# Optimization experiments

Hardware: AMD Instinct MI355X
Metric: run time of the kernel (lower is better)

## Reference

```python
import jax, jax.numpy as jnp
import numpy as np
from jax import lax

KS = [3, 3, 3, 5, 5, 7, 7, 7, 9, 9, 11, 11]  # deterministic sorted draw from [3,5,7,9,11], k=12
B, L, OUT_CH = 32, 262144, 4
EPS = 1e-5


def setup_inputs() -> dict:
    key = jax.random.key(0)
    ks = jax.random.split(key, 8 + len(KS))
    inp = {
        "x": jax.random.normal(ks[0], (B, 1, L), jnp.float32),
        "w1": jax.random.normal(ks[1], (128, 256), jnp.float32) * 0.0625,
        "b1": jnp.zeros((128,), jnp.float32),
        "w2": jax.random.normal(ks[2], (12, 128), jnp.float32) * 0.088,
        "b2": jnp.zeros((12,), jnp.float32),
        "bn_gamma": jnp.ones((OUT_CH,), jnp.float32),
        "bn_beta": jnp.zeros((OUT_CH,), jnp.float32),
    }
    for i, k in enumerate(KS):
        inp[f"k{i}"] = jax.random.normal(ks[8 + i], (OUT_CH, 1, k), jnp.float32)
    return inp


def reference(x, w1, b1, w2, b2, bn_gamma, bn_beta,
              k0, k1, k2, k3, k4, k5, k6, k7, k8, k9, k10, k11):
    kernels = [k0, k1, k2, k3, k4, k5, k6, k7, k8, k9, k10, k11]
    b, _, n = x.shape
    # Attention: AdaptiveAvgPool1d(256) -> Linear -> ReLU -> Linear -> softmax(dim=2)
    pooled = x.reshape(b, 1, 256, n // 256).mean(-1)            # [B,1,256]
    h = jax.nn.relu(jnp.einsum('bcd,hd->bch', pooled, w1) + b1)  # [B,1,128]
    y = jax.nn.softmax(jnp.einsum('bch,fh->bcf', h, w2) + b2, axis=2)  # [B,1,12]
    s = y[0, 0]  # scalar weight per filter (faithful to y[0][0][i] in source)

    max_len = n - KS[0] + 1
    out = jnp.zeros((b, OUT_CH, max_len), x.dtype)
    for i, k in enumerate(kernels):
        c = lax.conv_general_dilated(x, k * s[i], (1,), 'VALID',
                                     dimension_numbers=('NCH', 'OIH', 'NCH'))
        out = out.at[:, :, :c.shape[-1]].add(c)  # right-pad-with-zeros then add

    # BatchNorm1d in training mode: batch stats over (N, L), biased variance
    mean = out.mean(axis=(0, 2), keepdims=True)
    var = ((out - mean) ** 2).mean(axis=(0, 2), keepdims=True)
    out = (out - mean) * lax.rsqrt(var + EPS)
    out = out * bn_gamma[None, :, None] + bn_beta[None, :, None]
    return jax.nn.relu(out)
```

## Files before the change

kernel.cpp:

```cpp
#include <hip/hip_runtime.h>

#define L_LEN   262144
#define OUT_LEN 262142
#define BATCH   32
#define NTOT    (32.0 * 262142.0)

typedef float v4f __attribute__((ext_vector_type(4)));

struct KPtrs { const float* p[12]; };

__global__ void pool_kernel(const float* __restrict__ x, float* __restrict__ pooled) {
    int bin = blockIdx.x;
    int tid = threadIdx.x;
    const float4* x4 = (const float4*)(x + bin * 1024);
    float4 v = x4[tid];
    float sum = v.x + v.y + v.z + v.w;
    #pragma unroll
    for (int off = 32; off; off >>= 1) sum += __shfl_down(sum, off);
    __shared__ float wred[4];
    int wave = tid >> 6;
    if ((tid & 63) == 0) wred[wave] = sum;
    __syncthreads();
    if (tid == 0)
        pooled[bin] = (wred[0] + wred[1] + wred[2] + wred[3]) * (1.0f / 1024.0f);
}

__global__ __launch_bounds__(256, 4) void stats_mlp_kernel(const float* __restrict__ x,
                                                           const float* __restrict__ w1,
                                                           const float* __restrict__ b1,
                                                           const float* __restrict__ w2,
                                                           const float* __restrict__ b2,
                                                           KPtrs kp,
                                                           const float* __restrict__ pooled,
                                                           float* __restrict__ part,
                                                           float* __restrict__ Kraw) {
    int tid = threadIdx.x;

    if (blockIdx.x == 0) {
        __shared__ float h[128];
        __shared__ float logits[12];
        __shared__ float s[12];
        int w = tid >> 6, lane = tid & 63;
        float4 pv = ((const float4*)pooled)[lane];
        for (int i = 0; i < 32; ++i) {
            int t = w * 32 + i;
            float4 wv = ((const float4*)(w1 + t * 256))[lane];
            float p = wv.x * pv.x + wv.y * pv.y + wv.z * pv.z + wv.w * pv.w;
            #pragma unroll
            for (int off = 32; off; off >>= 1) p += __shfl_down(p, off);
            if (lane == 0) h[t] = fmaxf(p + b1[t], 0.0f);
        }
        __syncthreads();
        for (int f = w; f < 12; f += 4) {
            float2 wv = ((const float2*)(w2 + f * 128))[lane];
            float p = wv.x * h[2 * lane] + wv.y * h[2 * lane + 1];
            #pragma unroll
            for (int off = 32; off; off >>= 1) p += __shfl_down(p, off);
            if (lane == 0) logits[f] = p + b2[f];
        }
        __syncthreads();
        if (tid == 0) {
            float m = logits[0];
            #pragma unroll
            for (int i = 1; i < 12; ++i) m = fmaxf(m, logits[i]);
            float e[12]; float sum = 0.0f;
            #pragma unroll
            for (int i = 0; i < 12; ++i) { e[i] = expf(logits[i] - m); sum += e[i]; }
            float inv = 1.0f / sum;
            #pragma unroll
            for (int i = 0; i < 12; ++i) s[i] = e[i] * inv;
        }
        __syncthreads();
        constexpr int KSa[12] = {3,3,3,5,5,7,7,7,9,9,11,11};
        if (tid < 220) {
            int q = tid / 44, r = tid % 44, c = r / 11, j = r % 11;
            int kmax = 2 * q + 3;
            float v = 0.0f;
            #pragma unroll
            for (int i = 0; i < 12; ++i) {
                int k = KSa[i];
                if (k <= kmax && j < k) v = fmaf(s[i], kp.p[i][c * k + j], v);
            }
            Kraw[tid] = v;
        }
        return;
    }

    __shared__ float xt[2064];
    float X = 0.0f, R[11];
    #pragma unroll
    for (int l = 0; l < 11; ++l) R[l] = 0.0f;

    for (int it = 0; it < 4; ++it) {
        int T = (blockIdx.x - 1) * 4 + it;
        int row = T >> 7, seg = T & 127;
        int base = seg << 11;
        const float* xb = x + row * L_LEN;
        *(float4*)&xt[4 * tid]        = *(const float4*)(xb + base + 4 * tid);
        *(float4*)&xt[1024 + 4 * tid] = *(const float4*)(xb + base + 1024 + 4 * tid);
        if (tid < 3) {
            float4 v = {0.f, 0.f, 0.f, 0.f};
            if (seg < 127) v = *(const float4*)(xb + base + 2048 + 4 * tid);
            *(float4*)&xt[2048 + 4 * tid] = v;
        }
        __syncthreads();

        float xv[18];
        const float4* xr = (const float4*)&xt[8 * tid];
        #pragma unroll
        for (int i = 0; i < 4; ++i) {
            float4 a = xr[i];
            xv[4*i] = a.x; xv[4*i+1] = a.y; xv[4*i+2] = a.z; xv[4*i+3] = a.w;
        }
        float2 a4 = *(const float2*)&xt[8 * tid + 16];
        xv[16] = a4.x; xv[17] = a4.y;

        float s8 = 0.0f;
        #pragma unroll
        for (int p = 0; p < 8; ++p) s8 += xv[p];
        X += s8;
        #pragma unroll
        for (int l = 0; l < 11; ++l) {
            float r = 0.0f;
            #pragma unroll
            for (int p = 0; p < 8; ++p) r = fmaf(xv[p], xv[p + l], r);
            R[l] += r;
        }
        __syncthreads();
    }

    #pragma unroll
    for (int off = 32; off; off >>= 1) {
        X += __shfl_down(X, off);
        #pragma unroll
        for (int l = 0; l < 11; ++l) R[l] += __shfl_down(R[l], off);
    }
    __shared__ float red[4][12];
    int wave = tid >> 6;
    if ((tid & 63) == 0) {
        red[wave][0] = X;
        #pragma unroll
        for (int l = 0; l < 11; ++l) red[wave][1 + l] = R[l];
    }
    __syncthreads();
    if (tid < 12)
        part[tid * 1024 + (blockIdx.x - 1)] = red[0][tid] + red[1][tid] + red[2][tid] + red[3][tid];
}

__global__ void fold_kernel(const float* __restrict__ part,
                            const float* __restrict__ Kraw,
                            const float* __restrict__ gamma, const float* __restrict__ beta,
                            float* __restrict__ Kscl, float* __restrict__ biasv) {
    __shared__ double vals[12];
    __shared__ float Kr[220];
    __shared__ float g[4];
    int tid = threadIdx.x;
    int w = tid >> 6, lane = tid & 63;
    if (tid < 220) Kr[tid] = Kraw[tid];
    for (int v = w; v < 12; v += 4) {
        double d = 0.0;
        #pragma unroll 4
        for (int i = 0; i < 16; ++i) d += (double)part[v * 1024 + i * 64 + lane];
        #pragma unroll
        for (int off = 32; off; off >>= 1) d += __shfl_down(d, off);
        if (lane == 0) vals[v] = d;
    }
    __syncthreads();
    if (tid < 4) {
        int c = tid;
        const float* Kc = Kr + 4 * 44 + c * 11;
        double sK = 0.0;
        for (int j = 0; j < 11; ++j) sK += (double)Kc[j];
        double mean = sK * vals[0] / NTOT;
        double ex2 = 0.0;
        for (int l = 0; l < 11; ++l) {
            double A = 0.0;
            for (int j = 0; j + l < 11; ++j) A += (double)Kc[j] * (double)Kc[j + l];
            ex2 += (l ? 2.0 : 1.0) * A * vals[1 + l];
        }
        ex2 /= NTOT;
        double var = ex2 - mean * mean;
        float gg = gamma[c] * (float)(1.0 / sqrt(var + 1e-5));
        g[c] = gg;
        biasv[c] = beta[c] - (float)mean * gg;
    }
    __syncthreads();
    if (tid < 220) {
        int c = (tid / 11) % 4;
        Kscl[tid] = Kr[tid] * g[c];
    }
}

__global__ __launch_bounds__(256, 4) void write_kernel(const float* __restrict__ x,
                                                       const float* __restrict__ Kscl,
                                                       const float* __restrict__ biasv,
                                                       float* __restrict__ out) {
    __shared__ float xt[2064];
    int tid = threadIdx.x;
    int b = blockIdx.x >> 7, seg = blockIdx.x & 127;
    int base = seg << 11;
    const float* xb = x + b * L_LEN;

    *(float4*)&xt[4 * tid]        = *(const float4*)(xb + base + 4 * tid);
    *(float4*)&xt[1024 + 4 * tid] = *(const float4*)(xb + base + 1024 + 4 * tid);
    if (tid < 4) {
        float4 v = {0.f, 0.f, 0.f, 0.f};
        if (seg < 127) v = *(const float4*)(xb + base + 2048 + 4 * tid);
        *(float4*)&xt[2048 + 4 * tid] = v;
    }

    float K[4][11], bias[4];
    #pragma unroll
    for (int c = 0; c < 4; ++c) {
        #pragma unroll
        for (int j = 0; j < 11; ++j) K[c][j] = Kscl[4 * 44 + c * 11 + j];
        bias[c] = biasv[c];
    }
    __syncthreads();

    #pragma unroll
    for (int gdx = 0; gdx < 2; ++gdx) {
        int lt = gdx * 1024 + 4 * tid;
        bool scalar = (seg == 127) && (gdx == 1) && (tid >= 253);
        if (!scalar) {
            float xv[16];
            const float4* xr = (const float4*)&xt[lt];
            #pragma unroll
            for (int i = 0; i < 4; ++i) {
                float4 a = xr[i];
                xv[4*i] = a.x; xv[4*i+1] = a.y; xv[4*i+2] = a.z; xv[4*i+3] = a.w;
            }
            #pragma unroll
            for (int c = 0; c < 4; ++c) {
                int sh = (c & 1) ? 2 : 0;
                float v[4];
                #pragma unroll
                for (int p = 0; p < 4; ++p) {
                    float a = bias[c];
                    #pragma unroll
                    for (int j = 0; j < 11; ++j) a = fmaf(K[c][j], xv[sh + p + j], a);
                    v[p] = fmaxf(a, 0.0f);
                }
                float* op = out + (size_t)(4 * b + c) * OUT_LEN + base + sh + lt;
                *(v4f*)op = (v4f){v[0], v[1], v[2], v[3]};
            }
        } else {
            #pragma unroll
            for (int par = 0; par < 2; ++par) {
                int sh = 2 * par;
                for (int p = 0; p < 4; ++p) {
                    int t = base + sh + lt + p;
                    if (t >= OUT_LEN) continue;
                    int rem = L_LEN - t;
                    int q = (rem - 3) >> 1; if (q > 4) q = 4;
                    int kmax = 2 * q + 3;
                    int li = sh + lt + p;
                    for (int c = par; c < 4; c += 2) {
                        float a = bias[c];
                        for (int j = 0; j < kmax; ++j) a = fmaf(Kscl[q * 44 + c * 11 + j], xt[li + j], a);
                        out[(size_t)(4 * b + c) * OUT_LEN + t] = fmaxf(a, 0.0f);
                    }
                }
            }
        }
    }
    if (seg == 0 && tid == 0) {
        for (int c = 1; c < 4; c += 2) {
            for (int t = 0; t < 2; ++t) {
                float a = bias[c];
                #pragma unroll
                for (int j = 0; j < 11; ++j) a = fmaf(K[c][j], xt[t + j], a);
                out[(size_t)(4 * b + c) * OUT_LEN + t] = fmaxf(a, 0.0f);
            }
        }
    }
}

extern "C" void kernel_launch(void* const* d_in, const int* in_sizes, int n_in,
                              void* d_out, int out_size, void* d_ws, size_t ws_size,
                              hipStream_t stream) {
    const float* x     = (const float*)d_in[0];
    const float* w1    = (const float*)d_in[1];
    const float* b1    = (const float*)d_in[2];
    const float* w2    = (const float*)d_in[3];
    const float* b2    = (const float*)d_in[4];
    const float* gamma = (const float*)d_in[5];
    const float* beta  = (const float*)d_in[6];
    KPtrs kp;
    for (int i = 0; i < 12; ++i) kp.p[i] = (const float*)d_in[7 + i];
    float* out = (float*)d_out;

    char* ws = (char*)d_ws;
    float* pooled = (float*)(ws + 0);
    float* Kraw   = (float*)(ws + 1024);
    float* Kscl   = (float*)(ws + 2048);
    float* biasv  = (float*)(ws + 3072);
    float* part   = (float*)(ws + 4096);

    pool_kernel<<<dim3(256), dim3(256), 0, stream>>>(x, pooled);
    stats_mlp_kernel<<<dim3(1025), dim3(256), 0, stream>>>(x, w1, b1, w2, b2, kp,
                                                           pooled, part, Kraw);
    fold_kernel<<<dim3(1), dim3(256), 0, stream>>>(part, Kraw, gamma, beta, Kscl, biasv);
    write_kernel<<<dim3(4096), dim3(256), 0, stream>>>(x, Kscl, biasv, out);
}
```

Before: 80.84 us.

## Fuse pooling into MLP block and fold stats into persistent write kernel

Removes the separate pooling kernel by having block 0 of the stats kernel compute the 256 pooled bins itself, each thread serially summing 1024 floats. It also removes the single-block fold kernel: every write block now reduces the partial statistics and computes the BatchNorm scale and bias redundantly. The write kernel becomes persistent with 1024 blocks each handling four tiles. This cuts two launches and their serialization gaps, at the cost of a longer serial critical path in block 0 and redundant double-precision fold work in every block.

After: 108.6 us. +34.4%, slower.

```diff
diff --git a/kernel.cpp b/kernel.cpp
--- a/kernel.cpp
+++ b/kernel.cpp
@@ -2,28 +2,11 @@
 
 #define L_LEN   262144
 #define OUT_LEN 262142
-#define BATCH   32
 #define NTOT    (32.0 * 262142.0)
 
 typedef float v4f __attribute__((ext_vector_type(4)));
 
 struct KPtrs { const float* p[12]; };
-
-__global__ void pool_kernel(const float* __restrict__ x, float* __restrict__ pooled) {
-    int bin = blockIdx.x;
-    int tid = threadIdx.x;
-    const float4* x4 = (const float4*)(x + bin * 1024);
-    float4 v = x4[tid];
-    float sum = v.x + v.y + v.z + v.w;
-    #pragma unroll
-    for (int off = 32; off; off >>= 1) sum += __shfl_down(sum, off);
-    __shared__ float wred[4];
-    int wave = tid >> 6;
-    if ((tid & 63) == 0) wred[wave] = sum;
-    __syncthreads();
-    if (tid == 0)
-        pooled[bin] = (wred[0] + wred[1] + wred[2] + wred[3]) * (1.0f / 1024.0f);
-}
 
 __global__ __launch_bounds__(256, 4) void stats_mlp_kernel(const float* __restrict__ x,
                                                            const float* __restrict__ w1,
@@ -31,21 +14,32 @@
                                                            const float* __restrict__ w2,
                                                            const float* __restrict__ b2,
                                                            KPtrs kp,
-                                                           const float* __restrict__ pooled,
                                                            float* __restrict__ part,
                                                            float* __restrict__ Kraw) {
     int tid = threadIdx.x;
 
     if (blockIdx.x == 0) {
+        __shared__ float pooledL[256];
         __shared__ float h[128];
-        __shared__ float logits[12];
-        __shared__ float s[12];
+        __shared__ float lgt[12];
+        __shared__ float sm[12];
+        {
+            float s = 0.0f;
+            const float4* xq = (const float4*)(x + (size_t)1024 * tid);
+            #pragma unroll 8
+            for (int i = 0; i < 256; ++i) {
+                float4 v = xq[i];
+                s += (v.x + v.y) + (v.z + v.w);
+            }
+            pooledL[tid] = s * (1.0f / 1024.0f);
+        }
+        __syncthreads();
         int w = tid >> 6, lane = tid & 63;
-        float4 pv = ((const float4*)pooled)[lane];
+        float4 pv = *(const float4*)&pooledL[4 * lane];
         for (int i = 0; i < 32; ++i) {
             int t = w * 32 + i;
             float4 wv = ((const float4*)(w1 + t * 256))[lane];
-            float p = wv.x * pv.x + wv.y * pv.y + wv.z * pv.z + wv.w * pv.w;
+            float p = wv.x*pv.x + wv.y*pv.y + wv.z*pv.z + wv.w*pv.w;
             #pragma unroll
             for (int off = 32; off; off >>= 1) p += __shfl_down(p, off);
             if (lane == 0) h[t] = fmaxf(p + b1[t], 0.0f);
@@ -53,22 +47,22 @@
         __syncthreads();
         for (int f = w; f < 12; f += 4) {
             float2 wv = ((const float2*)(w2 + f * 128))[lane];
-            float p = wv.x * h[2 * lane] + wv.y * h[2 * lane + 1];
+            float p = wv.x * h[2*lane] + wv.y * h[2*lane + 1];
             #pragma unroll
             for (int off = 32; off; off >>= 1) p += __shfl_down(p, off);
-            if (lane == 0) logits[f] = p + b2[f];
+            if (lane == 0) lgt[f] = p + b2[f];
         }
         __syncthreads();
         if (tid == 0) {
-            float m = logits[0];
-            #pragma unroll
-            for (int i = 1; i < 12; ++i) m = fmaxf(m, logits[i]);
+            float m = lgt[0];
+            #pragma unroll
+            for (int i = 1; i < 12; ++i) m = fmaxf(m, lgt[i]);
             float e[12]; float sum = 0.0f;
             #pragma unroll
-            for (int i = 0; i < 12; ++i) { e[i] = expf(logits[i] - m); sum += e[i]; }
+            for (int i = 0; i < 12; ++i) { e[i] = expf(lgt[i] - m); sum += e[i]; }
             float inv = 1.0f / sum;
             #pragma unroll
-            for (int i = 0; i < 12; ++i) s[i] = e[i] * inv;
+            for (int i = 0; i < 12; ++i) sm[i] = e[i] * inv;
         }
         __syncthreads();
         constexpr int KSa[12] = {3,3,3,5,5,7,7,7,9,9,11,11};
@@ -79,7 +73,7 @@
             #pragma unroll
             for (int i = 0; i < 12; ++i) {
                 int k = KSa[i];
-                if (k <= kmax && j < k) v = fmaf(s[i], kp.p[i][c * k + j], v);
+                if (k <= kmax && j < k) v = fmaf(sm[i], kp.p[i][c * k + j], v);
             }
             Kraw[tid] = v;
         }
@@ -96,24 +90,24 @@
         int row = T >> 7, seg = T & 127;
         int base = seg << 11;
         const float* xb = x + row * L_LEN;
-        *(float4*)&xt[4 * tid]        = *(const float4*)(xb + base + 4 * tid);
-        *(float4*)&xt[1024 + 4 * tid] = *(const float4*)(xb + base + 1024 + 4 * tid);
+        *(float4*)&xt[4*tid]        = *(const float4*)(xb + base + 4*tid);
+        *(float4*)&xt[1024 + 4*tid] = *(const float4*)(xb + base + 1024 + 4*tid);
         if (tid < 3) {
-            float4 v = {0.f, 0.f, 0.f, 0.f};
-            if (seg < 127) v = *(const float4*)(xb + base + 2048 + 4 * tid);
-            *(float4*)&xt[2048 + 4 * tid] = v;
+            float4 v = {0.f,0.f,0.f,0.f};
+            if (seg < 127) v = *(const float4*)(xb + base + 2048 + 4*tid);
+            *(float4*)&xt[2048 + 4*tid] = v;
         }
         __syncthreads();
 
         float xv[18];
-        const float4* xr = (const float4*)&xt[8 * tid];
+        const float4* xr = (const float4*)&xt[8*tid];
         #pragma unroll
         for (int i = 0; i < 4; ++i) {
             float4 a = xr[i];
-            xv[4*i] = a.x; xv[4*i+1] = a.y; xv[4*i+2] = a.z; xv[4*i+3] = a.w;
-        }
-        float2 a4 = *(const float2*)&xt[8 * tid + 16];
-        xv[16] = a4.x; xv[17] = a4.y;
+            xv[4*i]=a.x; xv[4*i+1]=a.y; xv[4*i+2]=a.z; xv[4*i+3]=a.w;
+        }
+        float2 a4 = *(const float2*)&xt[8*tid + 16];
+        xv[16]=a4.x; xv[17]=a4.y;
 
         float s8 = 0.0f;
         #pragma unroll
@@ -123,7 +117,7 @@
         for (int l = 0; l < 11; ++l) {
             float r = 0.0f;
             #pragma unroll
-            for (int p = 0; p < 8; ++p) r = fmaf(xv[p], xv[p + l], r);
+            for (int p = 0; p < 8; ++p) r = fmaf(xv[p], xv[p+l], r);
             R[l] += r;
         }
         __syncthreads();
@@ -140,137 +134,132 @@
     if ((tid & 63) == 0) {
         red[wave][0] = X;
         #pragma unroll
-        for (int l = 0; l < 11; ++l) red[wave][1 + l] = R[l];
+        for (int l = 0; l < 11; ++l) red[wave][1+l] = R[l];
     }
     __syncthreads();
     if (tid < 12)
         part[tid * 1024 + (blockIdx.x - 1)] = red[0][tid] + red[1][tid] + red[2][tid] + red[3][tid];
 }
 
-__global__ void fold_kernel(const float* __restrict__ part,
-                            const float* __restrict__ Kraw,
-                            const float* __restrict__ gamma, const float* __restrict__ beta,
-                            float* __restrict__ Kscl, float* __restrict__ biasv) {
+__global__ __launch_bounds__(256, 4) void write_fold_kernel(const float* __restrict__ x,
+                                                            const float* __restrict__ Kraw,
+                                                            const float* __restrict__ part,
+                                                            const float* __restrict__ gamma,
+                                                            const float* __restrict__ beta,
+                                                            float* __restrict__ out) {
+    __shared__ float xt[2064];
     __shared__ double vals[12];
-    __shared__ float Kr[220];
-    __shared__ float g[4];
+    __shared__ float KrLds[220];
     int tid = threadIdx.x;
+    int blk = blockIdx.x;
     int w = tid >> 6, lane = tid & 63;
-    if (tid < 220) Kr[tid] = Kraw[tid];
+
+    if (tid < 220) KrLds[tid] = Kraw[tid];
     for (int v = w; v < 12; v += 4) {
         double d = 0.0;
         #pragma unroll 4
-        for (int i = 0; i < 16; ++i) d += (double)part[v * 1024 + i * 64 + lane];
+        for (int i = 0; i < 16; ++i) d += (double)part[v*1024 + i*64 + lane];
         #pragma unroll
         for (int off = 32; off; off >>= 1) d += __shfl_down(d, off);
         if (lane == 0) vals[v] = d;
     }
     __syncthreads();
-    if (tid < 4) {
-        int c = tid;
-        const float* Kc = Kr + 4 * 44 + c * 11;
-        double sK = 0.0;
-        for (int j = 0; j < 11; ++j) sK += (double)Kc[j];
-        double mean = sK * vals[0] / NTOT;
-        double ex2 = 0.0;
-        for (int l = 0; l < 11; ++l) {
-            double A = 0.0;
-            for (int j = 0; j + l < 11; ++j) A += (double)Kc[j] * (double)Kc[j + l];
-            ex2 += (l ? 2.0 : 1.0) * A * vals[1 + l];
-        }
-        ex2 /= NTOT;
-        double var = ex2 - mean * mean;
-        float gg = gamma[c] * (float)(1.0 / sqrt(var + 1e-5));
-        g[c] = gg;
-        biasv[c] = beta[c] - (float)mean * gg;
-    }
-    __syncthreads();
-    if (tid < 220) {
-        int c = (tid / 11) % 4;
-        Kscl[tid] = Kr[tid] * g[c];
-    }
-}
-
-__global__ __launch_bounds__(256, 4) void write_kernel(const float* __restrict__ x,
-                                                       const float* __restrict__ Kscl,
-                                                       const float* __restrict__ biasv,
-                                                       float* __restrict__ out) {
-    __shared__ float xt[2064];
-    int tid = threadIdx.x;
-    int b = blockIdx.x >> 7, seg = blockIdx.x & 127;
-    int base = seg << 11;
-    const float* xb = x + b * L_LEN;
-
-    *(float4*)&xt[4 * tid]        = *(const float4*)(xb + base + 4 * tid);
-    *(float4*)&xt[1024 + 4 * tid] = *(const float4*)(xb + base + 1024 + 4 * tid);
-    if (tid < 4) {
-        float4 v = {0.f, 0.f, 0.f, 0.f};
-        if (seg < 127) v = *(const float4*)(xb + base + 2048 + 4 * tid);
-        *(float4*)&xt[2048 + 4 * tid] = v;
-    }
-
-    float K[4][11], bias[4];
-    #pragma unroll
-    for (int c = 0; c < 4; ++c) {
-        #pragma unroll
-        for (int j = 0; j < 11; ++j) K[c][j] = Kscl[4 * 44 + c * 11 + j];
-        bias[c] = biasv[c];
-    }
-    __syncthreads();
-
-    #pragma unroll
-    for (int gdx = 0; gdx < 2; ++gdx) {
-        int lt = gdx * 1024 + 4 * tid;
-        bool scalar = (seg == 127) && (gdx == 1) && (tid >= 253);
-        if (!scalar) {
-            float xv[16];
-            const float4* xr = (const float4*)&xt[lt];
-            #pragma unroll
-            for (int i = 0; i < 4; ++i) {
-                float4 a = xr[i];
-                xv[4*i] = a.x; xv[4*i+1] = a.y; xv[4*i+2] = a.z; xv[4*i+3] = a.w;
-            }
-            #pragma unroll
-            for (int c = 0; c < 4; ++c) {
-                int sh = (c & 1) ? 2 : 0;
-                float v[4];
+
+    float Kt[4][11], bias[4], g[4];
+    {
+        const float* K44 = KrLds + 176;
+        double v0 = vals[0];
+        #pragma unroll
+        for (int c = 0; c < 4; ++c) {
+            double sK = 0.0;
+            for (int j = 0; j < 11; ++j) sK += (double)K44[c*11 + j];
+            double mean = sK * v0 / NTOT;
+            double ex2 = 0.0;
+            for (int l = 0; l < 11; ++l) {
+                double A = 0.0;
+                for (int j = 0; j + l < 11; ++j) A += (double)K44[c*11+j] * (double)K44[c*11+j+l];
+                ex2 += (l ? 2.0 : 1.0) * A * vals[1+l];
+            }
+            ex2 /= NTOT;
+            double var = ex2 - mean * mean;
+            float gg = gamma[c] * (float)(1.0 / sqrt(var + 1e-5));
+            g[c] = gg;
+            bias[c] = beta[c] - (float)mean * gg;
+            #pragma unroll
+            for (int j = 0; j < 11; ++j) Kt[c][j] = K44[c*11 + j] * gg;
+        }
+    }
+
+    for (int it = 0; it < 4; ++it) {
+        int T = it * 1024 + blk;
+        int b = T >> 7, seg = T & 127;
+        int base = seg << 11;
+        const float* xb = x + b * L_LEN;
+        __syncthreads();
+        *(float4*)&xt[4*tid]        = *(const float4*)(xb + base + 4*tid);
+        *(float4*)&xt[1024 + 4*tid] = *(const float4*)(xb + base + 1024 + 4*tid);
+        if (tid < 4) {
+            float4 v = {0.f,0.f,0.f,0.f};
+            if (seg < 127) v = *(const float4*)(xb + base + 2048 + 4*tid);
+            *(float4*)&xt[2048 + 4*tid] = v;
+        }
+        __syncthreads();
+
+        #pragma unroll
+        for (int gdx = 0; gdx < 2; ++gdx) {
+            int lt = gdx * 1024 + 4 * tid;
+            bool scalar = (seg == 127) && (gdx == 1) && (tid >= 253);
+            if (!scalar) {
+                float xv[16];
+                const float4* xr = (const float4*)&xt[lt];
                 #pragma unroll
-                for (int p = 0; p < 4; ++p) {
+                for (int i = 0; i < 4; ++i) {
+                    float4 a = xr[i];
+                    xv[4*i]=a.x; xv[4*i+1]=a.y; xv[4*i+2]=a.z; xv[4*i+3]=a.w;
+                }
+                #pragma unroll
+                for (int c = 0; c < 4; ++c) {
+                    int sh = (c & 1) ? 2 : 0;
+                    float v[4];
+                    #pragma unroll
+                    for (int p = 0; p < 4; ++p) {
+                        float a = bias[c];
+                        #pragma unroll
+                        for (int j = 0; j < 11; ++j) a = fmaf(Kt[c][j], xv[sh+p+j], a);
+                        v[p] = fmaxf(a, 0.0f);
+                    }
+                    float* op = out + (size_t)(4*b + c) * OUT_LEN + base + sh + lt;
+                    *(v4f*)op = (v4f){v[0], v[1], v[2], v[3]};
+                }
+            } else {
+                #pragma unroll
+                for (int par = 0; par < 2; ++par) {
+                    int sh = 2 * par;
+                    for (int p = 0; p < 4; ++p) {
+                        int t = base + sh + lt + p;
+                        if (t >= OUT_LEN) continue;
+                        int rem = L_LEN - t;
+                        int q = (rem - 3) >> 1; if (q > 4) q = 4;
+                        int kmax = 2 * q + 3;
+                        int li = sh + lt + p;
+                        for (int c = par; c < 4; c += 2) {
+                            float a = bias[c];
+                            for (int j = 0; j < kmax; ++j)
+                                a = fmaf(KrLds[q*44 + c*11 + j] * g[c], xt[li + j], a);
+                            out[(size_t)(4*b + c) * OUT_LEN + t] = fmaxf(a, 0.0f);
+                        }
+                    }
+                }
+            }
+        }
+        if (seg == 0 && tid == 0) {
+            for (int c = 1; c < 4; c += 2) {
+                for (int t = 0; t < 2; ++t) {
                     float a = bias[c];
                     #pragma unroll
-                    for (int j = 0; j < 11; ++j) a = fmaf(K[c][j], xv[sh + p + j], a);
-                    v[p] = fmaxf(a, 0.0f);
-                }
-                float* op = out + (size_t)(4 * b + c) * OUT_LEN + base + sh + lt;
-                *(v4f*)op = (v4f){v[0], v[1], v[2], v[3]};
-            }
-        } else {
-            #pragma unroll
-            for (int par = 0; par < 2; ++par) {
-                int sh = 2 * par;
-                for (int p = 0; p < 4; ++p) {
-                    int t = base + sh + lt + p;
-                    if (t >= OUT_LEN) continue;
-                    int rem = L_LEN - t;
-                    int q = (rem - 3) >> 1; if (q > 4) q = 4;
-                    int kmax = 2 * q + 3;
-                    int li = sh + lt + p;
-                    for (int c = par; c < 4; c += 2) {
-                        float a = bias[c];
-                        for (int j = 0; j < kmax; ++j) a = fmaf(Kscl[q * 44 + c * 11 + j], xt[li + j], a);
-                        out[(size_t)(4 * b + c) * OUT_LEN + t] = fmaxf(a, 0.0f);
-                    }
-                }
-            }
-        }
-    }
-    if (seg == 0 && tid == 0) {
-        for (int c = 1; c < 4; c += 2) {
-            for (int t = 0; t < 2; ++t) {
-                float a = bias[c];
-                #pragma unroll
-                for (int j = 0; j < 11; ++j) a = fmaf(K[c][j], xt[t + j], a);
-                out[(size_t)(4 * b + c) * OUT_LEN + t] = fmaxf(a, 0.0f);
+                    for (int j = 0; j < 11; ++j) a = fmaf(Kt[c][j], xt[t + j], a);
+                    out[(size_t)(4*b + c) * OUT_LEN + t] = fmaxf(a, 0.0f);
+                }
             }
         }
     }
@@ -291,15 +280,9 @@
     float* out = (float*)d_out;
 
     char* ws = (char*)d_ws;
-    float* pooled = (float*)(ws + 0);
-    float* Kraw   = (float*)(ws + 1024);
-    float* Kscl   = (float*)(ws + 2048);
-    float* biasv  = (float*)(ws + 3072);
-    float* part   = (float*)(ws + 4096);
-
-    pool_kernel<<<dim3(256), dim3(256), 0, stream>>>(x, pooled);
-    stats_mlp_kernel<<<dim3(1025), dim3(256), 0, stream>>>(x, w1, b1, w2, b2, kp,
-                                                           pooled, part, Kraw);
-    fold_kernel<<<dim3(1), dim3(256), 0, stream>>>(part, Kraw, gamma, beta, Kscl, biasv);
-    write_kernel<<<dim3(4096), dim3(256), 0, stream>>>(x, Kscl, biasv, out);
+    float* Kraw = (float*)(ws + 1024);
+    float* part = (float*)(ws + 4096);
+
+    stats_mlp_kernel<<<dim3(1025), dim3(256), 0, stream>>>(x, w1, b1, w2, b2, kp, part, Kraw);
+    write_fold_kernel<<<dim3(1024), dim3(256), 0, stream>>>(x, Kraw, part, gamma, beta, out);
 }
```
